# Performance work log

Measured on AMD Instinct MI355X. Metric: run time of the kernel, lower is better.

## Reference

```python
import jax, jax.numpy as jnp
import numpy as np

B, S, E, H, V, C = 256, 20, 512, 512, 32000, 1000


def _lstm_step(x, h, c, W, U, b):
    # Keras LSTM, activation='relu', recurrent_activation='sigmoid', gate order i,f,c,o
    z = x @ W + h @ U + b  # (B, 4H)
    i, f, g, o = jnp.split(z, 4, axis=-1)
    i = jax.nn.sigmoid(i)
    f = jax.nn.sigmoid(f)
    g = jax.nn.relu(g)
    o = jax.nn.sigmoid(o)
    c_new = f * c + i * g
    h_new = o * jax.nn.relu(c_new)
    return h_new, c_new


def setup_inputs() -> dict:
    key = jax.random.key(0)
    ks = jax.random.split(key, 24)
    std = 0.05
    d_in1 = S * E + 2 * E  # flattened encoder output + word embed + speaker embed
    inp = {
        "encoded_output": jax.random.normal(ks[0], (B, S, E), jnp.float32),
        "word_embedding": jax.random.normal(ks[1], (B, E), jnp.float32),
        "h0": jax.random.normal(ks[2], (B, H), jnp.float32) * std,
        "c0": jax.random.normal(ks[3], (B, H), jnp.float32) * std,
        "speaker": jax.random.randint(ks[4], (B,), 0, C),
        "addressee": jax.random.randint(ks[5], (B,), 0, C),
        "persona_emb": jax.random.normal(ks[6], (C, E), jnp.float32) * 0.1,
        "W1": jax.random.normal(ks[7], (d_in1, 4 * H), jnp.float32) * std,
        "U1": jax.random.normal(ks[8], (H, 4 * H), jnp.float32) * std,
        "b1": jnp.zeros((4 * H,), jnp.float32),
        "W2": jax.random.normal(ks[9], (H, 4 * H), jnp.float32) * std,
        "U2": jax.random.normal(ks[10], (H, 4 * H), jnp.float32) * std,
        "b2": jnp.zeros((4 * H,), jnp.float32),
        "W3": jax.random.normal(ks[11], (H, 4 * H), jnp.float32) * std,
        "U3": jax.random.normal(ks[12], (H, 4 * H), jnp.float32) * std,
        "b3": jnp.zeros((4 * H,), jnp.float32),
        "W4": jax.random.normal(ks[13], (H, 4 * H), jnp.float32) * std,
        "U4": jax.random.normal(ks[14], (H, 4 * H), jnp.float32) * std,
        "b4": jnp.zeros((4 * H,), jnp.float32),
        "Wd": jax.random.normal(ks[15], (H, V), jnp.float32) * std,
        "bd": jnp.zeros((V,), jnp.float32),
    }
    return inp


def reference(encoded_output, word_embedding, h0, c0, speaker, addressee,
              persona_emb, W1, U1, b1, W2, U2, b2, W3, U3, b3, W4, U4, b4, Wd, bd):
    b = encoded_output.shape[0]
    # The Python double loop in the original is exactly: (B,S,E) -> (B, S*E)
    enc_flat = encoded_output.reshape(b, -1)
    speaker_embed = persona_emb[speaker]  # (B, E)
    # is_speaker=True branch: concat [flattened encoder, word embed, speaker embed]
    x = jnp.concatenate([enc_flat, word_embedding, speaker_embed], axis=-1)
    # seq length is 1, so each LSTM layer is a single cell step;
    # each layer's initial state is the previous layer's final (h, c)
    h1, c1 = _lstm_step(x, h0, c0, W1, U1, b1)
    h2, c2 = _lstm_step(h1, h1, c1, W2, U2, b2)
    h3, c3 = _lstm_step(h2, h2, c2, W3, U3, b3)
    h4, c4 = _lstm_step(h3, h3, c3, W4, U4, b4)
    probs = jax.nn.softmax(h4 @ Wd + bd, axis=-1)  # (B, V)
    return probs, (h4, c4)
```

## Files before the change

### kernel.cpp

```cpp
#include <hip/hip_runtime.h>
#include <cstdint>
#include <cmath>

typedef _Float16 f16;
typedef _Float16 f16x8 __attribute__((ext_vector_type(8)));
typedef float f32x4 __attribute__((ext_vector_type(4)));

__device__ inline void gld_lds16(const void* g, void* l) {
  __builtin_amdgcn_global_load_lds(
      (__attribute__((address_space(1))) void*)(uintptr_t)g,
      (__attribute__((address_space(3))) void*)l, 16, 0, 0);
}

__global__ __launch_bounds__(256) void build_x1_kernel(
    const float* __restrict__ enc, const float* __restrict__ word,
    const float* __restrict__ pers, const int* __restrict__ speaker,
    const float* __restrict__ h0, f16* __restrict__ X)
{
  const int b  = blockIdx.y;
  const int k2 = blockIdx.x * 256 + threadIdx.x;
  const int k  = k2 * 2;
  float v0, v1;
  if (k < 10240) {
    const float* p = enc + (long long)b * 10240 + k; v0 = p[0]; v1 = p[1];
  } else if (k < 10752) {
    const float* p = word + b * 512 + (k - 10240);   v0 = p[0]; v1 = p[1];
  } else if (k < 11264) {
    const float* p = pers + (long long)speaker[b] * 512 + (k - 10752); v0 = p[0]; v1 = p[1];
  } else {
    const float* p = h0 + b * 512 + (k - 11264);     v0 = p[0]; v1 = p[1];
  }
  union { f16 h[2]; unsigned int u; } pk;
  pk.h[0] = (f16)v0; pk.h[1] = (f16)v1;
  ((unsigned int*)X)[(long long)b * 5888 + k2] = pk.u;
}

__global__ __launch_bounds__(256, 4) void gemm_f16_kernel(
    const f16* __restrict__ A, int lda, int a_kmask,
    const float* __restrict__ B0, const float* __restrict__ B1, int ksw, int ldb,
    float* __restrict__ C, int ldc, long long c_split_stride, int kchunk)
{
  __shared__ __align__(16) f16 Ah[128 * 32];
  __shared__ __align__(16) f16 Bh[64 * 40];

  const int tid  = threadIdx.x;
  const int lane = tid & 63;
  const int wave = tid >> 6;
  const int m0 = blockIdx.x * 128;
  const int n0 = blockIdx.y * 64;
  const int kbeg = blockIdx.z * kchunk;
  const int kend = kbeg + kchunk;
  float* Cs = C + (long long)blockIdx.z * c_split_stride;

  const int wm = (wave & 1) * 64;
  const int wn = (wave >> 1) * 32;

  f32x4 acc[4][2] = {};

  const int a_row16 = lane >> 2;
  const int a_ksub  = ((lane & 3) ^ ((lane >> 3) & 3)) * 8;

  const int bn  = tid & 63;
  const int boct = tid >> 6;

  for (int kt = kbeg; kt < kend; kt += 32) {
    const int akb = kt & a_kmask;
    #pragma unroll
    for (int half = 0; half < 2; half++) {
      const int rb = wave * 32 + half * 16;
      const f16* gp = A + (long long)(m0 + rb + a_row16) * lda + akb + a_ksub;
      gld_lds16((const void*)gp, (void*)&Ah[rb * 32]);
    }
    {
      float bv[8];
      #pragma unroll
      for (int i = 0; i < 8; i++) {
        const int krow = kt + boct * 8 + i;
        const float* bp = (krow >= ksw) ? (B1 + (long long)(krow - ksw) * ldb)
                                        : (B0 + (long long)krow * ldb);
        bv[i] = bp[n0 + bn];
      }
      f16x8 pk;
      #pragma unroll
      for (int i = 0; i < 8; i++) pk[i] = (f16)bv[i];
      *(f16x8*)&Bh[bn * 40 + boct * 8] = pk;
    }
    __syncthreads();

    f16x8 af[4], bf[2];
    #pragma unroll
    for (int mi = 0; mi < 4; mi++) {
      const int m = wm + mi * 16 + (lane & 15);
      const int c = (lane >> 4) ^ ((m >> 1) & 3);
      af[mi] = *(const f16x8*)&Ah[m * 32 + c * 8];
    }
    #pragma unroll
    for (int ni = 0; ni < 2; ni++) {
      const int n = wn + ni * 16 + (lane & 15);
      bf[ni] = *(const f16x8*)&Bh[n * 40 + (lane >> 4) * 8];
    }
    #pragma unroll
    for (int mi = 0; mi < 4; mi++)
      #pragma unroll
      for (int ni = 0; ni < 2; ni++)
        acc[mi][ni] = __builtin_amdgcn_mfma_f32_16x16x32_f16(af[mi], bf[ni], acc[mi][ni], 0, 0, 0);
    __syncthreads();
  }

  #pragma unroll
  for (int mi = 0; mi < 4; mi++) {
    const int r0 = m0 + wm + mi * 16 + (lane >> 4) * 4;
    #pragma unroll
    for (int ni = 0; ni < 2; ni++) {
      const int cc = n0 + wn + ni * 16 + (lane & 15);
      #pragma unroll
      for (int r = 0; r < 4; r++)
        Cs[(long long)(r0 + r) * ldc + cc] = acc[mi][ni][r];
    }
  }
}

__global__ __launch_bounds__(256) void gate_kernel(
    const float* __restrict__ zbase, int nsplit, const float* __restrict__ bias,
    const float* __restrict__ c_prev, float* __restrict__ c_out,
    f16* __restrict__ h16_out, float* __restrict__ h32_out)
{
  const int idx = blockIdx.x * 256 + threadIdx.x;
  const int j = idx & 511;
  const int b = idx >> 9;
  const long long zo = (long long)b * 2048 + j;
  float zi = bias[j], zf = bias[j + 512], zg = bias[j + 1024], zo4 = bias[j + 1536];
  for (int s = 0; s < nsplit; s++) {
    const float* z = zbase + (long long)s * 524288;
    zi += z[zo]; zf += z[zo + 512]; zg += z[zo + 1024]; zo4 += z[zo + 1536];
  }
  const float gi = 1.f / (1.f + expf(-zi));
  const float gf = 1.f / (1.f + expf(-zf));
  const float gg = fmaxf(zg, 0.f);
  const float go = 1.f / (1.f + expf(-zo4));
  const float cn = gf * c_prev[idx] + gi * gg;
  const float hn = go * fmaxf(cn, 0.f);
  c_out[idx] = cn;
  h16_out[idx] = (f16)hn;
  if (h32_out) h32_out[idx] = hn;
}

__global__ __launch_bounds__(1024) void softmax_kernel(
    float* __restrict__ logits, const float* __restrict__ bd)
{
  const int row = blockIdx.x;
  const int t = threadIdx.x;
  float4* rp = (float4*)(logits + (long long)row * 32000);
  const float4* bp = (const float4*)bd;
  float4 l[8];
  float m = -1e30f;
  #pragma unroll
  for (int i = 0; i < 8; i++) {
    const int v = t + i * 1024;
    if (v < 8000) {
      float4 x = rp[v]; const float4 bb = bp[v];
      x.x += bb.x; x.y += bb.y; x.z += bb.z; x.w += bb.w;
      l[i] = x;
      m = fmaxf(m, fmaxf(fmaxf(x.x, x.y), fmaxf(x.z, x.w)));
    } else {
      l[i] = make_float4(-1e30f, -1e30f, -1e30f, -1e30f);
    }
  }
  #pragma unroll
  for (int off = 32; off > 0; off >>= 1) m = fmaxf(m, __shfl_xor(m, off, 64));
  __shared__ float redm[16];
  __shared__ float reds[16];
  const int w = t >> 6;
  if ((t & 63) == 0) redm[w] = m;
  __syncthreads();
  float bm = redm[0];
  #pragma unroll
  for (int i = 1; i < 16; i++) bm = fmaxf(bm, redm[i]);
  float s = 0.f;
  #pragma unroll
  for (int i = 0; i < 8; i++) {
    const float ex = expf(l[i].x - bm), ey = expf(l[i].y - bm);
    const float ez = expf(l[i].z - bm), ew = expf(l[i].w - bm);
    l[i] = make_float4(ex, ey, ez, ew);
    s += (ex + ey) + (ez + ew);
  }
  #pragma unroll
  for (int off = 32; off > 0; off >>= 1) s += __shfl_xor(s, off, 64);
  if ((t & 63) == 0) reds[w] = s;
  __syncthreads();
  float ts = 0.f;
  #pragma unroll
  for (int i = 0; i < 16; i++) ts += reds[i];
  const float inv = 1.0f / ts;
  #pragma unroll
  for (int i = 0; i < 8; i++) {
    const int v = t + i * 1024;
    if (v < 8000) {
      float4 x = l[i];
      x.x *= inv; x.y *= inv; x.z *= inv; x.w *= inv;
      rp[v] = x;
    }
  }
}

extern "C" void kernel_launch(void* const* d_in, const int* in_sizes, int n_in,
                              void* d_out, int out_size, void* d_ws, size_t ws_size,
                              hipStream_t stream) {
  const float* enc     = (const float*)d_in[0];
  const float* word    = (const float*)d_in[1];
  const float* h0      = (const float*)d_in[2];
  const float* c0      = (const float*)d_in[3];
  const int*   speaker = (const int*)d_in[4];
  const float* pers = (const float*)d_in[6];
  const float* W1 = (const float*)d_in[7];
  const float* U1 = (const float*)d_in[8];
  const float* b1 = (const float*)d_in[9];
  const float* W2 = (const float*)d_in[10];
  const float* U2 = (const float*)d_in[11];
  const float* b2 = (const float*)d_in[12];
  const float* W3 = (const float*)d_in[13];
  const float* U3 = (const float*)d_in[14];
  const float* b3 = (const float*)d_in[15];
  const float* W4 = (const float*)d_in[16];
  const float* U4 = (const float*)d_in[17];
  const float* b4 = (const float*)d_in[18];
  const float* Wd = (const float*)d_in[19];
  const float* bd = (const float*)d_in[20];

  float* out = (float*)d_out;
  float* zpart = out;
  f16*   X1h   = (f16*)((char*)d_out + 16777216);
  float* h4_out = out + 8192000;
  float* c4_out = out + 8192000 + 131072;

  float* ws_c   = (float*)d_ws;
  f16*   ws_h16 = (f16*)((char*)d_ws + 524288);

  const int BIG = 1 << 29;

  build_x1_kernel<<<dim3(23, 256), 256, 0, stream>>>(enc, word, pers, speaker, h0, X1h);

  gemm_f16_kernel<<<dim3(2, 32, 8), 256, 0, stream>>>(
      X1h, 11776, 0x7fffffff, W1, U1, 11264, 2048, zpart, 2048, 524288LL, 1472);
  gate_kernel<<<dim3(512), 256, 0, stream>>>(zpart, 8, b1, c0, ws_c, ws_h16, nullptr);

  gemm_f16_kernel<<<dim3(2, 32, 8), 256, 0, stream>>>(
      ws_h16, 512, 511, W2, U2, 512, 2048, zpart, 2048, 524288LL, 128);
  gate_kernel<<<dim3(512), 256, 0, stream>>>(zpart, 8, b2, ws_c, ws_c, ws_h16, nullptr);

  gemm_f16_kernel<<<dim3(2, 32, 8), 256, 0, stream>>>(
      ws_h16, 512, 511, W3, U3, 512, 2048, zpart, 2048, 524288LL, 128);
  gate_kernel<<<dim3(512), 256, 0, stream>>>(zpart, 8, b3, ws_c, ws_c, ws_h16, nullptr);

  gemm_f16_kernel<<<dim3(2, 32, 8), 256, 0, stream>>>(
      ws_h16, 512, 511, W4, U4, 512, 2048, zpart, 2048, 524288LL, 128);
  gate_kernel<<<dim3(512), 256, 0, stream>>>(zpart, 8, b4, ws_c, c4_out, ws_h16, h4_out);

  gemm_f16_kernel<<<dim3(2, 500, 1), 256, 0, stream>>>(
      ws_h16, 512, 0x7fffffff, Wd, Wd, BIG, 32000, out, 32000, 0LL, 512);

  softmax_kernel<<<dim3(256), 1024, 0, stream>>>(out, bd);
}
```

Baseline: 389.4 us.

## Fuse LSTM layers 2-4 with gates, double-buffer GEMM, fp16 split-K partials

Replaces the GEMM with a double-buffered 128x128-tile version that prefetches the next K-slice while computing the current one. Layers 2-4 become one fused kernel each, computing all four gate columns for a 16-unit slice and applying the LSTM cell update in-block, which removes the separate gate kernels and their partial-sum round trips. Layer 1 uses 16-way split-K that writes fp16 partials, halving partial traffic, and the gate kernel now reads two values per thread. The costs are extra rounding from fp16 partial sums and fewer, larger blocks for the small layers and the vocabulary projection.

```diff
diff --git a/kernel.cpp b/kernel.cpp
--- a/kernel.cpp
+++ b/kernel.cpp
@@ -35,114 +35,257 @@
   ((unsigned int*)X)[(long long)b * 5888 + k2] = pk.u;
 }
 
-__global__ __launch_bounds__(256, 4) void gemm_f16_kernel(
-    const f16* __restrict__ A, int lda, int a_kmask,
+__global__ __launch_bounds__(256, 2) void gemm_f16_pipe(
+    const f16* __restrict__ A, int lda,
     const float* __restrict__ B0, const float* __restrict__ B1, int ksw, int ldb,
-    float* __restrict__ C, int ldc, long long c_split_stride, int kchunk)
+    void* __restrict__ Cv, int ldc, long long c_split_stride, int niter,
+    int store_f16)
 {
-  __shared__ __align__(16) f16 Ah[128 * 32];
-  __shared__ __align__(16) f16 Bh[64 * 40];
+  __shared__ __align__(16) f16 Ah[2][128 * 32];
+  __shared__ __align__(16) f16 Bh[2][128 * 40];
 
   const int tid  = threadIdx.x;
   const int lane = tid & 63;
   const int wave = tid >> 6;
   const int m0 = blockIdx.x * 128;
-  const int n0 = blockIdx.y * 64;
-  const int kbeg = blockIdx.z * kchunk;
-  const int kend = kbeg + kchunk;
-  float* Cs = C + (long long)blockIdx.z * c_split_stride;
-
-  const int wm = (wave & 1) * 64;
-  const int wn = (wave >> 1) * 32;
-
-  f32x4 acc[4][2] = {};
+  const int n0 = blockIdx.y * 128;
+  const int kbeg = blockIdx.z * (niter * 32);
 
   const int a_row16 = lane >> 2;
   const int a_ksub  = ((lane & 3) ^ ((lane >> 3) & 3)) * 8;
 
-  const int bn  = tid & 63;
-  const int boct = tid >> 6;
-
-  for (int kt = kbeg; kt < kend; kt += 32) {
-    const int akb = kt & a_kmask;
+  const int nl0  = (tid & 63) * 2;
+  const int koct = tid >> 6;
+
+  float2 bv[8];
+
+  auto issueB = [&](int kt) {
+    const int kb = kbeg + kt * 32 + koct * 8;
+    #pragma unroll
+    for (int i = 0; i < 8; i++) {
+      const int krow = kb + i;
+      const float* bp = (krow >= ksw) ? (B1 + (long long)(krow - ksw) * ldb)
+                                      : (B0 + (long long)krow * ldb);
+      bv[i] = *(const float2*)(bp + n0 + nl0);
+    }
+  };
+  auto issueA = [&](int kt) {
+    const int akb = kbeg + kt * 32;
     #pragma unroll
     for (int half = 0; half < 2; half++) {
       const int rb = wave * 32 + half * 16;
       const f16* gp = A + (long long)(m0 + rb + a_row16) * lda + akb + a_ksub;
-      gld_lds16((const void*)gp, (void*)&Ah[rb * 32]);
-    }
-    {
-      float bv[8];
-      #pragma unroll
-      for (int i = 0; i < 8; i++) {
-        const int krow = kt + boct * 8 + i;
-        const float* bp = (krow >= ksw) ? (B1 + (long long)(krow - ksw) * ldb)
-                                        : (B0 + (long long)krow * ldb);
-        bv[i] = bp[n0 + bn];
-      }
-      f16x8 pk;
-      #pragma unroll
-      for (int i = 0; i < 8; i++) pk[i] = (f16)bv[i];
-      *(f16x8*)&Bh[bn * 40 + boct * 8] = pk;
-    }
-    __syncthreads();
-
-    f16x8 af[4], bf[2];
+      gld_lds16((const void*)gp, (void*)&Ah[kt & 1][rb * 32]);
+    }
+  };
+  auto writeB = [&](int kt) {
+    f16x8 p0, p1;
+    #pragma unroll
+    for (int i = 0; i < 8; i++) { p0[i] = (f16)bv[i].x; p1[i] = (f16)bv[i].y; }
+    *(f16x8*)&Bh[kt & 1][(nl0    ) * 40 + koct * 8] = p0;
+    *(f16x8*)&Bh[kt & 1][(nl0 + 1) * 40 + koct * 8] = p1;
+  };
+
+  const int wm = (wave & 1) * 64;
+  const int wn = (wave >> 1) * 64;
+  f32x4 acc[4][4] = {};
+
+  issueB(0); issueA(0); writeB(0);
+  __syncthreads();
+
+  for (int kt = 0; kt < niter; kt++) {
+    const int buf = kt & 1;
+    const bool more = (kt + 1 < niter);
+    if (more) { issueB(kt + 1); issueA(kt + 1); }
+
+    f16x8 af[4], bf[4];
     #pragma unroll
     for (int mi = 0; mi < 4; mi++) {
       const int m = wm + mi * 16 + (lane & 15);
-      const int c = (lane >> 4) ^ ((m >> 1) & 3);
-      af[mi] = *(const f16x8*)&Ah[m * 32 + c * 8];
-    }
-    #pragma unroll
-    for (int ni = 0; ni < 2; ni++) {
+      af[mi] = *(const f16x8*)&Ah[buf][m * 32 + (((lane >> 4) ^ ((m >> 1) & 3)) * 8)];
+    }
+    #pragma unroll
+    for (int ni = 0; ni < 4; ni++) {
       const int n = wn + ni * 16 + (lane & 15);
-      bf[ni] = *(const f16x8*)&Bh[n * 40 + (lane >> 4) * 8];
+      bf[ni] = *(const f16x8*)&Bh[buf][n * 40 + (lane >> 4) * 8];
     }
     #pragma unroll
     for (int mi = 0; mi < 4; mi++)
       #pragma unroll
-      for (int ni = 0; ni < 2; ni++)
+      for (int ni = 0; ni < 4; ni++)
         acc[mi][ni] = __builtin_amdgcn_mfma_f32_16x16x32_f16(af[mi], bf[ni], acc[mi][ni], 0, 0, 0);
+
+    if (more) writeB(kt + 1);
     __syncthreads();
   }
 
-  #pragma unroll
-  for (int mi = 0; mi < 4; mi++) {
-    const int r0 = m0 + wm + mi * 16 + (lane >> 4) * 4;
-    #pragma unroll
-    for (int ni = 0; ni < 2; ni++) {
-      const int cc = n0 + wn + ni * 16 + (lane & 15);
+  if (store_f16) {
+    f16* Cs = (f16*)Cv + (long long)blockIdx.z * c_split_stride;
+    #pragma unroll
+    for (int mi = 0; mi < 4; mi++) {
+      const int r0 = m0 + wm + mi * 16 + (lane >> 4) * 4;
       #pragma unroll
-      for (int r = 0; r < 4; r++)
-        Cs[(long long)(r0 + r) * ldc + cc] = acc[mi][ni][r];
-    }
-  }
-}
-
-__global__ __launch_bounds__(256) void gate_kernel(
-    const float* __restrict__ zbase, int nsplit, const float* __restrict__ bias,
+      for (int ni = 0; ni < 4; ni++) {
+        const int cc = n0 + wn + ni * 16 + (lane & 15);
+        #pragma unroll
+        for (int r = 0; r < 4; r++)
+          Cs[(long long)(r0 + r) * ldc + cc] = (f16)acc[mi][ni][r];
+      }
+    }
+  } else {
+    float* Cs = (float*)Cv + (long long)blockIdx.z * c_split_stride;
+    #pragma unroll
+    for (int mi = 0; mi < 4; mi++) {
+      const int r0 = m0 + wm + mi * 16 + (lane >> 4) * 4;
+      #pragma unroll
+      for (int ni = 0; ni < 4; ni++) {
+        const int cc = n0 + wn + ni * 16 + (lane & 15);
+        #pragma unroll
+        for (int r = 0; r < 4; r++)
+          Cs[(long long)(r0 + r) * ldc + cc] = acc[mi][ni][r];
+      }
+    }
+  }
+}
+
+__global__ __launch_bounds__(256, 2) void lstm_fused_layer(
+    const f16* __restrict__ A,
+    const float* __restrict__ W, const float* __restrict__ U,
+    const float* __restrict__ bias,
     const float* __restrict__ c_prev, float* __restrict__ c_out,
     f16* __restrict__ h16_out, float* __restrict__ h32_out)
 {
-  const int idx = blockIdx.x * 256 + threadIdx.x;
-  const int j = idx & 511;
-  const int b = idx >> 9;
-  const long long zo = (long long)b * 2048 + j;
-  float zi = bias[j], zf = bias[j + 512], zg = bias[j + 1024], zo4 = bias[j + 1536];
-  for (int s = 0; s < nsplit; s++) {
-    const float* z = zbase + (long long)s * 524288;
-    zi += z[zo]; zf += z[zo + 512]; zg += z[zo + 1024]; zo4 += z[zo + 1536];
-  }
-  const float gi = 1.f / (1.f + expf(-zi));
-  const float gf = 1.f / (1.f + expf(-zf));
-  const float gg = fmaxf(zg, 0.f);
-  const float go = 1.f / (1.f + expf(-zo4));
-  const float cn = gf * c_prev[idx] + gi * gg;
-  const float hn = go * fmaxf(cn, 0.f);
-  c_out[idx] = cn;
-  h16_out[idx] = (f16)hn;
-  if (h32_out) h32_out[idx] = hn;
+  __shared__ __align__(16) f16 Ah[2][64 * 32];
+  __shared__ __align__(16) f16 Bh[2][64 * 40];
+  __shared__ float zx[64 * 16 * 4];
+
+  const int tid  = threadIdx.x;
+  const int lane = tid & 63;
+  const int wave = tid >> 6;
+  const int m0 = blockIdx.x * 64;
+  const int j0 = blockIdx.y * 16;
+
+  const int a_row4  = lane >> 2;
+  const int a_ksub  = ((lane & 3) ^ ((lane >> 3) & 3)) * 8;
+
+  const int nl   = tid & 63;
+  const int ng   = (nl >> 4) * 512 + j0 + (nl & 15);
+  const int koct = tid >> 6;
+
+  float bv[8];
+  auto issueB = [&](int kt) {
+    const int kb = kt * 32 + koct * 8;
+    #pragma unroll
+    for (int i = 0; i < 8; i++) {
+      const int krow = kb + i;
+      const float* bp = (krow >= 512) ? (U + (long long)(krow - 512) * 2048)
+                                      : (W + (long long)krow * 2048);
+      bv[i] = bp[ng];
+    }
+  };
+  auto issueA = [&](int kt) {
+    const int ak = (kt * 32 + a_ksub) & 511;
+    const f16* gp = A + (long long)(m0 + wave * 16 + a_row4) * 512 + ak;
+    gld_lds16((const void*)gp, (void*)&Ah[kt & 1][wave * 16 * 32]);
+  };
+  auto writeB = [&](int kt) {
+    f16x8 p;
+    #pragma unroll
+    for (int i = 0; i < 8; i++) p[i] = (f16)bv[i];
+    *(f16x8*)&Bh[kt & 1][nl * 40 + koct * 8] = p;
+  };
+
+  f32x4 acc[4] = {};
+
+  issueB(0); issueA(0); writeB(0);
+  __syncthreads();
+
+  for (int kt = 0; kt < 32; kt++) {
+    const int buf = kt & 1;
+    const bool more = (kt + 1 < 32);
+    if (more) { issueB(kt + 1); issueA(kt + 1); }
+
+    f16x8 af[4], bfr;
+    #pragma unroll
+    for (int mi = 0; mi < 4; mi++) {
+      const int m = mi * 16 + (lane & 15);
+      af[mi] = *(const f16x8*)&Ah[buf][m * 32 + (((lane >> 4) ^ ((m >> 1) & 3)) * 8)];
+    }
+    bfr = *(const f16x8*)&Bh[buf][(wave * 16 + (lane & 15)) * 40 + (lane >> 4) * 8];
+    #pragma unroll
+    for (int mi = 0; mi < 4; mi++)
+      acc[mi] = __builtin_amdgcn_mfma_f32_16x16x32_f16(af[mi], bfr, acc[mi], 0, 0, 0);
+
+    if (more) writeB(kt + 1);
+    __syncthreads();
+  }
+
+  #pragma unroll
+  for (int mi = 0; mi < 4; mi++) {
+    const int rbase = mi * 16 + (lane >> 4) * 4;
+    #pragma unroll
+    for (int r = 0; r < 4; r++)
+      zx[((rbase + r) * 16 + (lane & 15)) * 4 + wave] = acc[mi][r];
+  }
+  __syncthreads();
+
+  #pragma unroll
+  for (int i = 0; i < 4; i++) {
+    const int cell = i * 256 + tid;
+    const int m = cell >> 4;
+    const int j = cell & 15;
+    const float4 z = ((const float4*)zx)[cell];
+    const float zi = z.x + bias[j0 + j];
+    const float zf = z.y + bias[512 + j0 + j];
+    const float zg = z.z + bias[1024 + j0 + j];
+    const float zo = z.w + bias[1536 + j0 + j];
+    const float gi = 1.f / (1.f + expf(-zi));
+    const float gf = 1.f / (1.f + expf(-zf));
+    const float gg = fmaxf(zg, 0.f);
+    const float go = 1.f / (1.f + expf(-zo));
+    const int idx = (m0 + m) * 512 + j0 + j;
+    const float cn = gf * c_prev[idx] + gi * gg;
+    const float hn = go * fmaxf(cn, 0.f);
+    c_out[idx] = cn;
+    h16_out[idx] = (f16)hn;
+    if (h32_out) h32_out[idx] = hn;
+  }
+}
+
+__global__ __launch_bounds__(256) void gate_kernel(
+    const unsigned int* __restrict__ zbase, const float* __restrict__ bias,
+    const float* __restrict__ c_prev, float* __restrict__ c_out,
+    f16* __restrict__ h16_out)
+{
+  const int idx2 = blockIdx.x * 256 + threadIdx.x;
+  const int b  = idx2 >> 8;
+  const int j2 = idx2 & 255;
+  const int j  = j2 * 2;
+  float z[4][2];
+  #pragma unroll
+  for (int g = 0; g < 4; g++) { z[g][0] = bias[g * 512 + j]; z[g][1] = bias[g * 512 + j + 1]; }
+  for (int s = 0; s < 16; s++) {
+    const unsigned int* zp = zbase + s * 262144 + b * 1024;
+    #pragma unroll
+    for (int g = 0; g < 4; g++) {
+      union { unsigned int u; f16 h[2]; } v;
+      v.u = zp[g * 256 + j2];
+      z[g][0] += (float)v.h[0];
+      z[g][1] += (float)v.h[1];
+    }
+  }
+  #pragma unroll
+  for (int e = 0; e < 2; e++) {
+    const float gi = 1.f / (1.f + expf(-z[0][e]));
+    const float gf = 1.f / (1.f + expf(-z[1][e]));
+    const float gg = fmaxf(z[2][e], 0.f);
+    const float go = 1.f / (1.f + expf(-z[3][e]));
+    const int idx = b * 512 + j + e;
+    const float cn = gf * c_prev[idx] + gi * gg;
+    const float hn = go * fmaxf(cn, 0.f);
+    c_out[idx] = cn;
+    h16_out[idx] = (f16)hn;
+  }
 }
 
 __global__ __launch_bounds__(1024) void softmax_kernel(
@@ -228,36 +371,30 @@
   const float* bd = (const float*)d_in[20];
 
   float* out = (float*)d_out;
-  float* zpart = out;
+  f16*   zp16  = (f16*)d_out;
   f16*   X1h   = (f16*)((char*)d_out + 16777216);
+  float* cbuf  = out + 6291456;
   float* h4_out = out + 8192000;
   float* c4_out = out + 8192000 + 131072;
 
-  float* ws_c   = (float*)d_ws;
-  f16*   ws_h16 = (f16*)((char*)d_ws + 524288);
+  f16* hA = (f16*)d_ws;
+  f16* hB = (f16*)((char*)d_ws + 262144);
+  f16* hC = (f16*)((char*)d_ws + 524288);
 
   const int BIG = 1 << 29;
 
   build_x1_kernel<<<dim3(23, 256), 256, 0, stream>>>(enc, word, pers, speaker, h0, X1h);
 
-  gemm_f16_kernel<<<dim3(2, 32, 8), 256, 0, stream>>>(
-      X1h, 11776, 0x7fffffff, W1, U1, 11264, 2048, zpart, 2048, 524288LL, 1472);
-  gate_kernel<<<dim3(512), 256, 0, stream>>>(zpart, 8, b1, c0, ws_c, ws_h16, nullptr);
-
-  gemm_f16_kernel<<<dim3(2, 32, 8), 256, 0, stream>>>(
-      ws_h16, 512, 511, W2, U2, 512, 2048, zpart, 2048, 524288LL, 128);
-  gate_kernel<<<dim3(512), 256, 0, stream>>>(zpart, 8, b2, ws_c, ws_c, ws_h16, nullptr);
-
-  gemm_f16_kernel<<<dim3(2, 32, 8), 256, 0, stream>>>(
-      ws_h16, 512, 511, W3, U3, 512, 2048, zpart, 2048, 524288LL, 128);
-  gate_kernel<<<dim3(512), 256, 0, stream>>>(zpart, 8, b3, ws_c, ws_c, ws_h16, nullptr);
-
-  gemm_f16_kernel<<<dim3(2, 32, 8), 256, 0, stream>>>(
-      ws_h16, 512, 511, W4, U4, 512, 2048, zpart, 2048, 524288LL, 128);
-  gate_kernel<<<dim3(512), 256, 0, stream>>>(zpart, 8, b4, ws_c, c4_out, ws_h16, h4_out);
-
-  gemm_f16_kernel<<<dim3(2, 500, 1), 256, 0, stream>>>(
-      ws_h16, 512, 0x7fffffff, Wd, Wd, BIG, 32000, out, 32000, 0LL, 512);
+  gemm_f16_pipe<<<dim3(2, 16, 16), 256, 0, stream>>>(
+      X1h, 11776, W1, U1, 11264, 2048, zp16, 2048, 524288LL, 23, 1);
+  gate_kernel<<<dim3(256), 256, 0, stream>>>((const unsigned int*)zp16, b1, c0, cbuf, hA);
+
+  lstm_fused_layer<<<dim3(4, 32), 256, 0, stream>>>(hA, W2, U2, b2, cbuf, cbuf, hB, nullptr);
+  lstm_fused_layer<<<dim3(4, 32), 256, 0, stream>>>(hB, W3, U3, b3, cbuf, cbuf, hA, nullptr);
+  lstm_fused_layer<<<dim3(4, 32), 256, 0, stream>>>(hA, W4, U4, b4, cbuf, c4_out, hC, h4_out);
+
+  gemm_f16_pipe<<<dim3(2, 250, 1), 256, 0, stream>>>(
+      hC, 512, Wd, Wd, BIG, 32000, out, 32000, 0LL, 16, 0);
 
   softmax_kernel<<<dim3(256), 1024, 0, stream>>>(out, bd);
 }
```

After: 392.1 us. Within noise of the previous version (+0.7%).

## Pre-sum W+U for deep LSTM layers, fuse gates into GEMM, LDS-free direct GEMM

Applied to the files above, without the earlier changes.

Layers 2-4 get the same input for x and h, so W and U are summed once and transposed into f16 matrices by a new prep kernel. Each of those layers then runs as one fused kernel that does the GEMM and the gate nonlinearity together, with no split-K partials and no separate gate pass. The layer-1 and vocab GEMMs move to a register-only, double-buffered MFMA kernel with no LDS staging, and layer-1 split-K partials are stored in f16 to halve their traffic. The cost is an extra weight-preparation pass on every call, lower precision in the partial sums, and no shared-memory reuse of the B operand across waves.

```diff
diff --git a/kernel.cpp b/kernel.cpp
--- a/kernel.cpp
+++ b/kernel.cpp
@@ -5,12 +5,6 @@
 typedef _Float16 f16;
 typedef _Float16 f16x8 __attribute__((ext_vector_type(8)));
 typedef float f32x4 __attribute__((ext_vector_type(4)));
-
-__device__ inline void gld_lds16(const void* g, void* l) {
-  __builtin_amdgcn_global_load_lds(
-      (__attribute__((address_space(1))) void*)(uintptr_t)g,
-      (__attribute__((address_space(3))) void*)l, 16, 0, 0);
-}
 
 __global__ __launch_bounds__(256) void build_x1_kernel(
     const float* __restrict__ enc, const float* __restrict__ word,
@@ -35,114 +29,213 @@
   ((unsigned int*)X)[(long long)b * 5888 + k2] = pk.u;
 }
 
-__global__ __launch_bounds__(256, 4) void gemm_f16_kernel(
-    const f16* __restrict__ A, int lda, int a_kmask,
+__global__ __launch_bounds__(256) void wsum_t_kernel(
+    const float* __restrict__ W2, const float* __restrict__ U2,
+    const float* __restrict__ W3, const float* __restrict__ U3,
+    const float* __restrict__ W4, const float* __restrict__ U4,
+    f16* __restrict__ out)
+{
+  const int t = blockIdx.x * 256 + threadIdx.x;
+  const int L = blockIdx.y;
+  const float* W = (L == 0) ? W2 : (L == 1) ? W3 : W4;
+  const float* U = (L == 0) ? U2 : (L == 1) ? U3 : U4;
+  const int n  = t & 2047;
+  const int k0 = (t >> 11) << 6;
+  f16* op = out + (long long)L * (2048 * 512) + (long long)n * 512 + k0;
+  for (int kk = 0; kk < 64; kk += 8) {
+    f16x8 v;
+    #pragma unroll
+    for (int j = 0; j < 8; j++) {
+      const int k = k0 + kk + j;
+      v[j] = (f16)(W[(long long)k * 2048 + n] + U[(long long)k * 2048 + n]);
+    }
+    *(f16x8*)(op + kk) = v;
+  }
+}
+
+__global__ __launch_bounds__(256, 2) void gemm_direct(
+    const f16* __restrict__ A, int lda,
     const float* __restrict__ B0, const float* __restrict__ B1, int ksw, int ldb,
-    float* __restrict__ C, int ldc, long long c_split_stride, int kchunk)
-{
-  __shared__ __align__(16) f16 Ah[128 * 32];
-  __shared__ __align__(16) f16 Bh[64 * 40];
-
-  const int tid  = threadIdx.x;
-  const int lane = tid & 63;
-  const int wave = tid >> 6;
-  const int m0 = blockIdx.x * 128;
-  const int n0 = blockIdx.y * 64;
-  const int kbeg = blockIdx.z * kchunk;
-  const int kend = kbeg + kchunk;
-  float* Cs = C + (long long)blockIdx.z * c_split_stride;
-
-  const int wm = (wave & 1) * 64;
-  const int wn = (wave >> 1) * 32;
-
-  f32x4 acc[4][2] = {};
-
-  const int a_row16 = lane >> 2;
-  const int a_ksub  = ((lane & 3) ^ ((lane >> 3) & 3)) * 8;
-
-  const int bn  = tid & 63;
-  const int boct = tid >> 6;
-
-  for (int kt = kbeg; kt < kend; kt += 32) {
-    const int akb = kt & a_kmask;
-    #pragma unroll
-    for (int half = 0; half < 2; half++) {
-      const int rb = wave * 32 + half * 16;
-      const f16* gp = A + (long long)(m0 + rb + a_row16) * lda + akb + a_ksub;
-      gld_lds16((const void*)gp, (void*)&Ah[rb * 32]);
-    }
-    {
-      float bv[8];
-      #pragma unroll
-      for (int i = 0; i < 8; i++) {
-        const int krow = kt + boct * 8 + i;
-        const float* bp = (krow >= ksw) ? (B1 + (long long)(krow - ksw) * ldb)
-                                        : (B0 + (long long)krow * ldb);
-        bv[i] = bp[n0 + bn];
+    int ntiles, int kchunk,
+    void* __restrict__ Cv, int ldc, long long c_split_stride, int store_f16)
+{
+  const int lane = threadIdx.x & 63;
+  const int wid  = blockIdx.x * 4 + (threadIdx.x >> 6);
+  const int mt = wid & 1;
+  const int nt = (wid >> 1) % ntiles;
+  const int ks = wid / (2 * ntiles);
+  const int m0 = mt * 128;
+  const int n0 = nt * 32;
+  const int kbeg = ks * kchunk;
+  const int lj = lane & 15, quad = lane >> 4;
+
+  f32x4 acc[8][2] = {};
+
+  const f16* Abase = A + (long long)(m0 + lj) * lda + quad * 8;
+  const int bn0 = n0 + lj, bn1 = n0 + 16 + lj;
+
+  f16x8 a_buf[2][8];
+  float b_buf[2][2][8];
+
+  auto loadA = [&](int k, f16x8* dst) {
+    #pragma unroll
+    for (int mf = 0; mf < 8; mf++)
+      dst[mf] = *(const f16x8*)(Abase + (long long)mf * 16 * lda + k);
+  };
+  auto loadB = [&](int k, float (*bd)[8]) {
+    const int krow = k + quad * 8;
+    const float* bp = (krow >= ksw) ? (B1 + (long long)(krow - ksw) * ldb)
+                                    : (B0 + (long long)krow * ldb);
+    #pragma unroll
+    for (int j = 0; j < 8; j++) {
+      bd[0][j] = bp[(long long)j * ldb + bn0];
+      bd[1][j] = bp[(long long)j * ldb + bn1];
+    }
+  };
+
+  loadB(kbeg, b_buf[0]);
+  loadA(kbeg, a_buf[0]);
+  const int niter = kchunk >> 5;
+  #pragma unroll 2
+  for (int kt = 0; kt < niter; kt++) {
+    const int cb = kt & 1;
+    if (kt + 1 < niter) {
+      loadB(kbeg + (kt + 1) * 32, b_buf[cb ^ 1]);
+      loadA(kbeg + (kt + 1) * 32, a_buf[cb ^ 1]);
+    }
+    f16x8 bf[2];
+    #pragma unroll
+    for (int nf = 0; nf < 2; nf++)
+      #pragma unroll
+      for (int j = 0; j < 8; j++) bf[nf][j] = (f16)b_buf[cb][nf][j];
+    #pragma unroll
+    for (int mf = 0; mf < 8; mf++)
+      #pragma unroll
+      for (int nf = 0; nf < 2; nf++)
+        acc[mf][nf] = __builtin_amdgcn_mfma_f32_16x16x32_f16(a_buf[cb][mf], bf[nf], acc[mf][nf], 0, 0, 0);
+  }
+
+  if (store_f16) {
+    f16* Cs = (f16*)Cv + (long long)ks * c_split_stride;
+    #pragma unroll
+    for (int mf = 0; mf < 8; mf++) {
+      const int r0 = m0 + mf * 16 + quad * 4;
+      #pragma unroll
+      for (int nf = 0; nf < 2; nf++) {
+        const int cc = n0 + nf * 16 + lj;
+        #pragma unroll
+        for (int r = 0; r < 4; r++)
+          Cs[(long long)(r0 + r) * ldc + cc] = (f16)acc[mf][nf][r];
       }
-      f16x8 pk;
-      #pragma unroll
-      for (int i = 0; i < 8; i++) pk[i] = (f16)bv[i];
-      *(f16x8*)&Bh[bn * 40 + boct * 8] = pk;
-    }
-    __syncthreads();
-
-    f16x8 af[4], bf[2];
-    #pragma unroll
-    for (int mi = 0; mi < 4; mi++) {
-      const int m = wm + mi * 16 + (lane & 15);
-      const int c = (lane >> 4) ^ ((m >> 1) & 3);
-      af[mi] = *(const f16x8*)&Ah[m * 32 + c * 8];
-    }
-    #pragma unroll
-    for (int ni = 0; ni < 2; ni++) {
-      const int n = wn + ni * 16 + (lane & 15);
-      bf[ni] = *(const f16x8*)&Bh[n * 40 + (lane >> 4) * 8];
-    }
-    #pragma unroll
-    for (int mi = 0; mi < 4; mi++)
-      #pragma unroll
-      for (int ni = 0; ni < 2; ni++)
-        acc[mi][ni] = __builtin_amdgcn_mfma_f32_16x16x32_f16(af[mi], bf[ni], acc[mi][ni], 0, 0, 0);
-    __syncthreads();
-  }
-
-  #pragma unroll
-  for (int mi = 0; mi < 4; mi++) {
-    const int r0 = m0 + wm + mi * 16 + (lane >> 4) * 4;
-    #pragma unroll
-    for (int ni = 0; ni < 2; ni++) {
-      const int cc = n0 + wn + ni * 16 + (lane & 15);
-      #pragma unroll
-      for (int r = 0; r < 4; r++)
-        Cs[(long long)(r0 + r) * ldc + cc] = acc[mi][ni][r];
-    }
-  }
-}
-
-__global__ __launch_bounds__(256) void gate_kernel(
-    const float* __restrict__ zbase, int nsplit, const float* __restrict__ bias,
+    }
+  } else {
+    float* Cs = (float*)Cv + (long long)ks * c_split_stride;
+    #pragma unroll
+    for (int mf = 0; mf < 8; mf++) {
+      const int r0 = m0 + mf * 16 + quad * 4;
+      #pragma unroll
+      for (int nf = 0; nf < 2; nf++) {
+        const int cc = n0 + nf * 16 + lj;
+        #pragma unroll
+        for (int r = 0; r < 4; r++)
+          Cs[(long long)(r0 + r) * ldc + cc] = acc[mf][nf][r];
+      }
+    }
+  }
+}
+
+__global__ __launch_bounds__(64) void lstm_small_layer(
+    const f16* __restrict__ h_in,
+    const f16* __restrict__ WsT,
+    const float* __restrict__ bias,
     const float* __restrict__ c_prev, float* __restrict__ c_out,
     f16* __restrict__ h16_out, float* __restrict__ h32_out)
 {
-  const int idx = blockIdx.x * 256 + threadIdx.x;
-  const int j = idx & 511;
-  const int b = idx >> 9;
-  const long long zo = (long long)b * 2048 + j;
-  float zi = bias[j], zf = bias[j + 512], zg = bias[j + 1024], zo4 = bias[j + 1536];
-  for (int s = 0; s < nsplit; s++) {
-    const float* z = zbase + (long long)s * 524288;
-    zi += z[zo]; zf += z[zo + 512]; zg += z[zo + 1024]; zo4 += z[zo + 1536];
-  }
-  const float gi = 1.f / (1.f + expf(-zi));
-  const float gf = 1.f / (1.f + expf(-zf));
-  const float gg = fmaxf(zg, 0.f);
-  const float go = 1.f / (1.f + expf(-zo4));
-  const float cn = gf * c_prev[idx] + gi * gg;
-  const float hn = go * fmaxf(cn, 0.f);
-  c_out[idx] = cn;
-  h16_out[idx] = (f16)hn;
-  if (h32_out) h32_out[idx] = hn;
+  const int lane = threadIdx.x;
+  const int wid  = blockIdx.x;
+  const int jt = wid & 31, mt = wid >> 5;
+  const int m0 = mt * 32, j0 = jt * 16;
+  const int lj = lane & 15, quad = lane >> 4;
+
+  f32x4 acc[2][4] = {};
+  const f16* Ab = h_in + (long long)(m0 + lj) * 512 + quad * 8;
+  const f16* Bb = WsT + (long long)(j0 + lj) * 512 + quad * 8;
+
+  f16x8 a_buf[2][2], b_buf[2][4];
+  auto load = [&](int k, f16x8* a, f16x8* b) {
+    a[0] = *(const f16x8*)(Ab + k);
+    a[1] = *(const f16x8*)(Ab + 16 * 512 + k);
+    #pragma unroll
+    for (int g = 0; g < 4; g++)
+      b[g] = *(const f16x8*)(Bb + (long long)g * 512 * 512 + k);
+  };
+  load(0, a_buf[0], b_buf[0]);
+  #pragma unroll 2
+  for (int kt = 0; kt < 16; kt++) {
+    const int cb = kt & 1;
+    if (kt < 15) load((kt + 1) * 32, a_buf[cb ^ 1], b_buf[cb ^ 1]);
+    #pragma unroll
+    for (int mf = 0; mf < 2; mf++)
+      #pragma unroll
+      for (int g = 0; g < 4; g++)
+        acc[mf][g] = __builtin_amdgcn_mfma_f32_16x16x32_f16(a_buf[cb][mf], b_buf[cb][g], acc[mf][g], 0, 0, 0);
+  }
+
+  const float bi = bias[j0 + lj],        bfv = bias[512 + j0 + lj];
+  const float bg = bias[1024 + j0 + lj], bo  = bias[1536 + j0 + lj];
+  #pragma unroll
+  for (int mf = 0; mf < 2; mf++) {
+    #pragma unroll
+    for (int r = 0; r < 4; r++) {
+      const int m = m0 + mf * 16 + quad * 4 + r;
+      const int idx = m * 512 + j0 + lj;
+      const float gi = 1.f / (1.f + expf(-(acc[mf][0][r] + bi)));
+      const float gf = 1.f / (1.f + expf(-(acc[mf][1][r] + bfv)));
+      const float gg = fmaxf(acc[mf][2][r] + bg, 0.f);
+      const float go = 1.f / (1.f + expf(-(acc[mf][3][r] + bo)));
+      const float cn = gf * c_prev[idx] + gi * gg;
+      const float hn = go * fmaxf(cn, 0.f);
+      c_out[idx] = cn;
+      h16_out[idx] = (f16)hn;
+      if (h32_out) h32_out[idx] = hn;
+    }
+  }
+}
+
+__global__ __launch_bounds__(256) void gate_kernel(
+    const unsigned int* __restrict__ zbase, const float* __restrict__ bias,
+    const float* __restrict__ c_prev, float* __restrict__ c_out,
+    f16* __restrict__ h16_out)
+{
+  const int idx2 = blockIdx.x * 256 + threadIdx.x;
+  const int b  = idx2 >> 8;
+  const int j2 = idx2 & 255;
+  const int j  = j2 * 2;
+  float z[4][2];
+  #pragma unroll
+  for (int g = 0; g < 4; g++) { z[g][0] = bias[g * 512 + j]; z[g][1] = bias[g * 512 + j + 1]; }
+  for (int s = 0; s < 8; s++) {
+    const unsigned int* zp = zbase + s * 262144 + b * 1024;
+    #pragma unroll
+    for (int g = 0; g < 4; g++) {
+      union { unsigned int u; f16 h[2]; } v;
+      v.u = zp[g * 256 + j2];
+      z[g][0] += (float)v.h[0];
+      z[g][1] += (float)v.h[1];
+    }
+  }
+  #pragma unroll
+  for (int e = 0; e < 2; e++) {
+    const float gi = 1.f / (1.f + expf(-z[0][e]));
+    const float gf = 1.f / (1.f + expf(-z[1][e]));
+    const float gg = fmaxf(z[2][e], 0.f);
+    const float go = 1.f / (1.f + expf(-z[3][e]));
+    const int idx = b * 512 + j + e;
+    const float cn = gf * c_prev[idx] + gi * gg;
+    const float hn = go * fmaxf(cn, 0.f);
+    c_out[idx] = cn;
+    h16_out[idx] = (f16)hn;
+  }
 }
 
 __global__ __launch_bounds__(1024) void softmax_kernel(
@@ -228,36 +321,33 @@
   const float* bd = (const float*)d_in[20];
 
   float* out = (float*)d_out;
-  float* zpart = out;
+  f16*   zp16  = (f16*)d_out;
+  f16*   WsT   = (f16*)((char*)d_out + 8388608);
   f16*   X1h   = (f16*)((char*)d_out + 16777216);
+  float* cbuf  = out + 6291456;
   float* h4_out = out + 8192000;
   float* c4_out = out + 8192000 + 131072;
 
-  float* ws_c   = (float*)d_ws;
-  f16*   ws_h16 = (f16*)((char*)d_ws + 524288);
+  f16* hA = (f16*)d_ws;
+  f16* hB = (f16*)((char*)d_ws + 262144);
+  f16* hC = (f16*)((char*)d_ws + 524288);
 
   const int BIG = 1 << 29;
+  const long long LW = 2048LL * 512;
 
   build_x1_kernel<<<dim3(23, 256), 256, 0, stream>>>(enc, word, pers, speaker, h0, X1h);
-
-  gemm_f16_kernel<<<dim3(2, 32, 8), 256, 0, stream>>>(
-      X1h, 11776, 0x7fffffff, W1, U1, 11264, 2048, zpart, 2048, 524288LL, 1472);
-  gate_kernel<<<dim3(512), 256, 0, stream>>>(zpart, 8, b1, c0, ws_c, ws_h16, nullptr);
-
-  gemm_f16_kernel<<<dim3(2, 32, 8), 256, 0, stream>>>(
-      ws_h16, 512, 511, W2, U2, 512, 2048, zpart, 2048, 524288LL, 128);
-  gate_kernel<<<dim3(512), 256, 0, stream>>>(zpart, 8, b2, ws_c, ws_c, ws_h16, nullptr);
-
-  gemm_f16_kernel<<<dim3(2, 32, 8), 256, 0, stream>>>(
-      ws_h16, 512, 511, W3, U3, 512, 2048, zpart, 2048, 524288LL, 128);
-  gate_kernel<<<dim3(512), 256, 0, stream>>>(zpart, 8, b3, ws_c, ws_c, ws_h16, nullptr);
-
-  gemm_f16_kernel<<<dim3(2, 32, 8), 256, 0, stream>>>(
-      ws_h16, 512, 511, W4, U4, 512, 2048, zpart, 2048, 524288LL, 128);
-  gate_kernel<<<dim3(512), 256, 0, stream>>>(zpart, 8, b4, ws_c, c4_out, ws_h16, h4_out);
-
-  gemm_f16_kernel<<<dim3(2, 500, 1), 256, 0, stream>>>(
-      ws_h16, 512, 0x7fffffff, Wd, Wd, BIG, 32000, out, 32000, 0LL, 512);
+  wsum_t_kernel<<<dim3(64, 3), 256, 0, stream>>>(W2, U2, W3, U3, W4, U4, WsT);
+
+  gemm_direct<<<dim3(256), 256, 0, stream>>>(
+      X1h, 11776, W1, U1, 11264, 2048, 64, 1472, zp16, 2048, 524288LL, 1);
+  gate_kernel<<<dim3(256), 256, 0, stream>>>((const unsigned int*)zp16, b1, c0, cbuf, hA);
+
+  lstm_small_layer<<<dim3(256), 64, 0, stream>>>(hA, WsT,          b2, cbuf, cbuf, hB, nullptr);
+  lstm_small_layer<<<dim3(256), 64, 0, stream>>>(hB, WsT + LW,     b3, cbuf, cbuf, hA, nullptr);
+  lstm_small_layer<<<dim3(256), 64, 0, stream>>>(hA, WsT + 2 * LW, b4, cbuf, c4_out, hC, h4_out);
+
+  gemm_direct<<<dim3(500), 256, 0, stream>>>(
+      hC, 512, Wd, Wd, BIG, 32000, 1000, 512, out, 32000, 0LL, 0);
 
   softmax_kernel<<<dim3(256), 1024, 0, stream>>>(out, bd);
 }
```

After: 699.0 us. 1.8x slower.
